# Kernel tuning notes

Hardware: AMD Instinct MI355X
Metric: run time of the kernel (lower is better)

The kernel has to match this reference:

```python
import jax, jax.numpy as jnp
import numpy as np

B, N, D = 8, 1024, 768
H = 12
HD = D // H  # 64
SCALE = HD ** (-0.5)


def setup_inputs() -> dict:
    key = jax.random.key(0)
    ks = jax.random.split(key, 11)
    s = 0.02
    return {
        "x": jax.random.normal(ks[0], (B, N, D), dtype=jnp.float32),
        "w_q": jax.random.normal(ks[1], (D, D), dtype=jnp.float32) * s,
        "b_q": jax.random.normal(ks[2], (D,), dtype=jnp.float32) * s,
        "w_k": jax.random.normal(ks[3], (D, D), dtype=jnp.float32) * s,
        "b_k": jax.random.normal(ks[4], (D,), dtype=jnp.float32) * s,
        "w_v": jax.random.normal(ks[5], (D, D), dtype=jnp.float32) * s,
        "b_v": jax.random.normal(ks[6], (D,), dtype=jnp.float32) * s,
        "w_qt": jax.random.normal(ks[7], (D, D), dtype=jnp.float32) * s,
        "b_qt": jax.random.normal(ks[8], (D,), dtype=jnp.float32) * s,
        "w_p": jax.random.normal(ks[9], (D, D), dtype=jnp.float32) * s,
        "b_p": jax.random.normal(ks[10], (D,), dtype=jnp.float32) * s,
    }


def _heads(y):
    # [B,N,D] -> [B,H,N,HD]
    b, n, d = y.shape
    return y.reshape(b, n, H, HD).transpose(0, 2, 1, 3)


def reference(x, w_q, b_q, w_k, b_k, w_v, b_v, w_qt, b_qt, w_p, b_p):
    # torch nn.Linear: y = x @ W.T + b
    q = _heads(x @ w_q.T + b_q)
    k = _heads(x @ w_k.T + b_k)
    v = _heads(x @ w_v.T + b_v)
    q_tilde = _heads(x @ w_qt.T + b_qt)
    # NOTE: source divides by self.scale = head_dim**-0.5 (i.e. multiplies by sqrt(hd)); reproduced faithfully
    corr = jnp.einsum("bhnd,bhmd->bhnm", q_tilde, k) / SCALE
    scores = jnp.einsum("bhnd,bhmd->bhnm", q, k) / SCALE + corr
    attn = jax.nn.softmax(scores, axis=-1)
    out = jnp.einsum("bhnm,bhmd->bhnd", attn, v)  # [B,H,N,HD]
    out = out.transpose(0, 2, 1, 3).reshape(x.shape[0], x.shape[1], D)
    out = out @ w_p.T + b_p
    return out, corr
```

## Files before the change

### kernel.cpp

```cpp
#include <hip/hip_runtime.h>

typedef __bf16 bf16_t;
typedef __bf16 bf16x8 __attribute__((ext_vector_type(8)));
typedef __bf16 bf16x4 __attribute__((ext_vector_type(4)));
typedef float f32x4 __attribute__((ext_vector_type(4)));

constexpr int BATCH = 8;
constexpr int NSEQ = 1024;
constexpr int DMODEL = 768;
constexpr int NH = 12;
constexpr int HDIM = 64;
constexpr int MROWS = BATCH * NSEQ;
constexpr int WSZ = DMODEL * DMODEL;
constexpr float L2E = 1.44269504088896f;

#define AS1(p) ((const __attribute__((address_space(1))) void*)(p))
#define AS3(p) ((__attribute__((address_space(3))) void*)(p))

__global__ __launch_bounds__(256) void prep_w(
    const float* __restrict__ wq, const float* __restrict__ wqt,
    const float* __restrict__ wk, const float* __restrict__ wv,
    const float* __restrict__ wp, const float* __restrict__ bq,
    const float* __restrict__ bqt, ushort* __restrict__ wb_,
    float* __restrict__ bqs)
{
    int i = blockIdx.x * 256 + threadIdx.x;
    bf16_t* w = (bf16_t*)wb_;
    float a = wq[i], b = wqt[i];
    w[i]            = (bf16_t)(a + b);
    w[WSZ + i]      = (bf16_t)b;
    w[2*WSZ + i]    = (bf16_t)wk[i];
    w[3*WSZ + i]    = (bf16_t)wv[i];
    w[4*WSZ + i]    = (bf16_t)wp[i];
    if (i < DMODEL) bqs[i] = bq[i] + bqt[i];
}

__global__ __launch_bounds__(256) void conv_x(const float* __restrict__ x,
                                              ushort* __restrict__ xb_)
{
    int i = (blockIdx.x * 256 + threadIdx.x) * 4;
    float4 v = *(const float4*)(x + i);
    bf16x4 r = { (bf16_t)v.x, (bf16_t)v.y, (bf16_t)v.z, (bf16_t)v.w };
    *(bf16x4*)((bf16_t*)xb_ + i) = r;
}

__device__ __forceinline__ void gemm_core(
    const bf16_t* __restrict__ A, const bf16_t* __restrict__ W,
    bf16_t* As, bf16_t* Bs, int m0, int n0, int tid, f32x4 acc[4][4])
{
    const int lane = tid & 63, wave = tid >> 6;
    const int g = lane >> 4, c = lane & 15;
    const int wm = wave >> 1, wn = wave & 1;

    const int r_b = tid >> 3;
    const int koff = 8 * ((tid & 7) ^ (r_b & 7));
    const size_t arow = (size_t)(m0 + r_b) * DMODEL + koff;
    const size_t brow = (size_t)(n0 + r_b) * DMODEL + koff;
    char* As_base = (char*)As + (tid & ~63) * 16;
    char* Bs_base = (char*)Bs + (tid & ~63) * 16;

    for (int k0 = 0; k0 < DMODEL; k0 += 64) {
        __syncthreads();
#pragma unroll
        for (int i = 0; i < 4; i++)
            __builtin_amdgcn_global_load_lds(
                AS1(A + arow + k0 + (size_t)i * 32 * DMODEL),
                AS3(As_base + i * 4096), 16, 0, 0);
#pragma unroll
        for (int i = 0; i < 4; i++)
            __builtin_amdgcn_global_load_lds(
                AS1(W + brow + k0 + (size_t)i * 32 * DMODEL),
                AS3(Bs_base + i * 4096), 16, 0, 0);
        __syncthreads();
#pragma unroll
        for (int kk = 0; kk < 2; kk++) {
            bf16x8 af[4], bfr[4];
#pragma unroll
            for (int mt = 0; mt < 4; mt++) {
                int r = wm * 64 + mt * 16 + c;
                af[mt] = *(const bf16x8*)(As + r * 64 + ((kk * 4 + g) ^ (r & 7)) * 8);
            }
#pragma unroll
            for (int nt = 0; nt < 4; nt++) {
                int r = wn * 64 + nt * 16 + c;
                bfr[nt] = *(const bf16x8*)(Bs + r * 64 + ((kk * 4 + g) ^ (r & 7)) * 8);
            }
#pragma unroll
            for (int mt = 0; mt < 4; mt++)
#pragma unroll
                for (int nt = 0; nt < 4; nt++)
                    acc[mt][nt] = __builtin_amdgcn_mfma_f32_16x16x32_bf16(
                        af[mt], bfr[nt], acc[mt][nt], 0, 0, 0);
        }
    }
}

__global__ __launch_bounds__(256) void gemm_qkv(
    const ushort* __restrict__ xb_, const ushort* __restrict__ wb_,
    const float* __restrict__ bqs, const float* __restrict__ bqt,
    const float* __restrict__ bk, const float* __restrict__ bv,
    ushort* __restrict__ o0, ushort* __restrict__ o1,
    ushort* __restrict__ o2, ushort* __restrict__ o3)
{
    __shared__ alignas(16) bf16_t As[128 * 64];
    __shared__ alignas(16) bf16_t Bs[128 * 64];
    const int bid = blockIdx.x;
    const int gid = (bid & 7) * 192 + (bid >> 3);
    const int z = gid / 384;
    const int rr = gid % 384;
    const int m0 = (rr / 6) * 128, n0 = (rr % 6) * 128;

    const bf16_t* A = (const bf16_t*)xb_;
    const bf16_t* W = (const bf16_t*)wb_ + (size_t)z * WSZ;
    const float* bias = (z == 0) ? bqs : (z == 1) ? bqt : (z == 2) ? bk : bv;
    bf16_t* outp = (bf16_t*)((z == 0) ? o0 : (z == 1) ? o1 : (z == 2) ? o2 : o3);
    f32x4 acc[4][4] = {};
    gemm_core(A, W, As, Bs, m0, n0, threadIdx.x, acc);

    const int tid = threadIdx.x, lane = tid & 63, wave = tid >> 6;
    const int g = lane >> 4, c = lane & 15;
    const int wm = wave >> 1, wn = wave & 1;
#pragma unroll
    for (int mt = 0; mt < 4; mt++)
#pragma unroll
        for (int nt = 0; nt < 4; nt++) {
            int col = n0 + wn * 64 + nt * 16 + c;
            int h = col >> 6, hd = col & 63;
            float bsv = bias[col];
#pragma unroll
            for (int j = 0; j < 4; j++) {
                int row = m0 + wm * 64 + mt * 16 + 4 * g + j;
                int b = row >> 10, ns = row & 1023;
                outp[(((size_t)b * NH + h) * NSEQ + ns) * HDIM + hd] =
                    (bf16_t)(acc[mt][nt][j] + bsv);
            }
        }
}

__global__ __launch_bounds__(256) void gemm_out(
    const ushort* __restrict__ ao_, const ushort* __restrict__ wp_,
    const float* __restrict__ bp, float* __restrict__ out)
{
    __shared__ alignas(16) bf16_t As[128 * 64];
    __shared__ alignas(16) bf16_t Bs[128 * 64];
    const int bid = blockIdx.x;
    const int gid = (bid & 7) * 48 + (bid >> 3);
    const int m0 = (gid / 6) * 128, n0 = (gid % 6) * 128;

    const bf16_t* A = (const bf16_t*)ao_;
    const bf16_t* W = (const bf16_t*)wp_;
    f32x4 acc[4][4] = {};
    gemm_core(A, W, As, Bs, m0, n0, threadIdx.x, acc);

    const int tid = threadIdx.x, lane = tid & 63, wave = tid >> 6;
    const int g = lane >> 4, c = lane & 15;
    const int wm = wave >> 1, wn = wave & 1;
#pragma unroll
    for (int mt = 0; mt < 4; mt++)
#pragma unroll
        for (int nt = 0; nt < 4; nt++) {
            int col = n0 + wn * 64 + nt * 16 + c;
            float bsv = bp[col];
#pragma unroll
            for (int j = 0; j < 4; j++) {
                int row = m0 + wm * 64 + mt * 16 + 4 * g + j;
                out[(size_t)row * DMODEL + col] = acc[mt][nt][j] + bsv;
            }
        }
}

__global__ __launch_bounds__(256) void attn_kernel(
    const ushort* __restrict__ qs_, const ushort* __restrict__ qt_,
    const ushort* __restrict__ kb_, const ushort* __restrict__ vb_,
    ushort* __restrict__ ao_, float* __restrict__ corr)
{
    __shared__ alignas(16) bf16_t VT[2][64 * 64];
    __shared__ alignas(16) bf16_t P[4][16 * 72];
    const bf16_t* QS = (const bf16_t*)qs_;
    const bf16_t* QT = (const bf16_t*)qt_;
    const bf16_t* Kb = (const bf16_t*)kb_;
    const bf16_t* Vb = (const bf16_t*)vb_;
    bf16_t* Ob = (bf16_t*)ao_;

    const int tid = threadIdx.x;
    const int w = tid >> 6, lane = tid & 63;
    const int g = lane >> 4, c = lane & 15;
    const int bid = blockIdx.x;
    const int gid = (bid & 7) * 192 + (bid >> 3);
    const int bh = gid >> 4, qb = gid & 15;
    const int q0 = qb * 64 + w * 16;
    const size_t base = (size_t)bh * (NSEQ * HDIM);

    bf16x8 qsf[2], qtf[2];
#pragma unroll
    for (int kk = 0; kk < 2; kk++) {
        qsf[kk] = *(const bf16x8*)(QS + base + (size_t)(q0 + c) * HDIM + kk * 32 + 8 * g);
        qtf[kk] = *(const bf16x8*)(QT + base + (size_t)(q0 + c) * HDIM + kk * 32 + 8 * g);
    }
    f32x4 oacc[4] = {};
    float mrun = -3e30f, lrun = 0.f;

    float* corr_b = corr + (size_t)bh * (NSEQ * NSEQ);
    float* corr_row = corr_b + (size_t)(q0 + c) * NSEQ + 4 * g;
    f32x4 ca_hold[4];

    for (int t = 0; t < 16; t++) {
        const int kv0 = t * 64;
        bf16_t* vt = VT[t & 1];
#pragma unroll
        for (int r2 = 0; r2 < 2; r2++) {
            const int hd0 = (r2 * 4 + w) * 8;
            bf16x8 vv = *(const bf16x8*)(Vb + base + (size_t)(kv0 + lane) * HDIM + hd0);
#pragma unroll
            for (int e = 0; e < 8; e++) {
                const int hd = hd0 + e;
                vt[hd * 64 + (lane ^ ((hd & 7) << 3))] = vv[e];
            }
        }
        bf16x8 kf[4][2];
#pragma unroll
        for (int kvt = 0; kvt < 4; kvt++) {
            const size_t krow = base + (size_t)(kv0 + kvt * 16 + c) * HDIM + 8 * g;
            kf[kvt][0] = *(const bf16x8*)(Kb + krow);
            kf[kvt][1] = *(const bf16x8*)(Kb + krow + 32);
        }
        if (t) {
#pragma unroll
            for (int kvt = 0; kvt < 4; kvt++)
                *(f32x4*)(corr_row + (kv0 - 64) + kvt * 16) = ca_hold[kvt];
        }
        f32x4 sv[4];
#pragma unroll
        for (int kvt = 0; kvt < 4; kvt++) {
            f32x4 sa = {0.f, 0.f, 0.f, 0.f};
            f32x4 ca = {0.f, 0.f, 0.f, 0.f};
            sa = __builtin_amdgcn_mfma_f32_16x16x32_bf16(kf[kvt][0], qsf[0], sa, 0, 0, 0);
            sa = __builtin_amdgcn_mfma_f32_16x16x32_bf16(kf[kvt][1], qsf[1], sa, 0, 0, 0);
            ca = __builtin_amdgcn_mfma_f32_16x16x32_bf16(kf[kvt][0], qtf[0], ca, 0, 0, 0);
            ca = __builtin_amdgcn_mfma_f32_16x16x32_bf16(kf[kvt][1], qtf[1], ca, 0, 0, 0);
            sv[kvt] = sa * 8.0f;
            ca_hold[kvt] = ca * 8.0f;
        }
        f32x4 mm;
#pragma unroll
        for (int j = 0; j < 4; j++)
            mm[j] = fmaxf(fmaxf(sv[0][j], sv[1][j]), fmaxf(sv[2][j], sv[3][j]));
        float tm = fmaxf(fmaxf(mm[0], mm[1]), fmaxf(mm[2], mm[3]));
        tm = fmaxf(tm, __shfl_xor(tm, 16));
        tm = fmaxf(tm, __shfl_xor(tm, 32));
        if (__any(tm > mrun + 8.0f)) {
            float newm = fmaxf(mrun, tm);
            float scl = exp2f((mrun - newm) * L2E);
            mrun = newm;
            lrun *= scl;
#pragma unroll
            for (int j = 0; j < 4; j++) {
                float scj = __shfl(scl, 4 * g + j);
#pragma unroll
                for (int nt = 0; nt < 4; nt++) oacc[nt][j] *= scj;
            }
        }
        float ps = 0.f;
#pragma unroll
        for (int kvt = 0; kvt < 4; kvt++)
#pragma unroll
            for (int j = 0; j < 4; j++) {
                float p = exp2f((sv[kvt][j] - mrun) * L2E);
                sv[kvt][j] = p;
                ps += p;
            }
        ps += __shfl_xor(ps, 16);
        ps += __shfl_xor(ps, 32);
        lrun += ps;
#pragma unroll
        for (int kvt = 0; kvt < 4; kvt++) {
            bf16x4 pb = { (bf16_t)sv[kvt][0], (bf16_t)sv[kvt][1],
                          (bf16_t)sv[kvt][2], (bf16_t)sv[kvt][3] };
            *(bf16x4*)(&P[w][c * 72 + kvt * 16 + 4 * g]) = pb;
        }
        asm volatile("s_waitcnt lgkmcnt(0)" ::: "memory");
        __builtin_amdgcn_sched_barrier(0);
        __builtin_amdgcn_s_barrier();
#pragma unroll
        for (int kk = 0; kk < 2; kk++) {
            bf16x8 pa = *(const bf16x8*)(&P[w][c * 72 + kk * 32 + 8 * g]);
#pragma unroll
            for (int nt = 0; nt < 4; nt++) {
                const int hd = nt * 16 + c;
                bf16x8 vf = *(const bf16x8*)(&vt[hd * 64 + ((kk * 32 + 8 * g) ^ ((hd & 7) << 3))]);
                oacc[nt] = __builtin_amdgcn_mfma_f32_16x16x32_bf16(pa, vf, oacc[nt], 0, 0, 0);
            }
        }
    }
#pragma unroll
    for (int kvt = 0; kvt < 4; kvt++)
        *(f32x4*)(corr_row + 960 + kvt * 16) = ca_hold[kvt];
    const int b = bh / NH, h = bh % NH;
    float lj[4];
#pragma unroll
    for (int j = 0; j < 4; j++) lj[j] = __shfl(lrun, 4 * g + j);
#pragma unroll
    for (int nt = 0; nt < 4; nt++)
#pragma unroll
        for (int j = 0; j < 4; j++) {
            float val = oacc[nt][j] / lj[j];
            Ob[(size_t)(b * NSEQ + q0 + 4 * g + j) * DMODEL + h * HDIM + nt * 16 + c] =
                (bf16_t)val;
        }
}

extern "C" void kernel_launch(void* const* d_in, const int* in_sizes, int n_in,
                              void* d_out, int out_size, void* d_ws, size_t ws_size,
                              hipStream_t stream)
{
    const float* x   = (const float*)d_in[0];
    const float* wq  = (const float*)d_in[1];
    const float* bq  = (const float*)d_in[2];
    const float* wk  = (const float*)d_in[3];
    const float* bk  = (const float*)d_in[4];
    const float* wv  = (const float*)d_in[5];
    const float* bv  = (const float*)d_in[6];
    const float* wqt = (const float*)d_in[7];
    const float* bqt = (const float*)d_in[8];
    const float* wp  = (const float*)d_in[9];
    const float* bp  = (const float*)d_in[10];

    char* ws = (char*)d_ws;
    ushort* xb  = (ushort*)(ws);
    ushort* wb  = (ushort*)(ws + 12582912);
    float*  bqs = (float*)(ws + 18481152);
    ushort* qs  = (ushort*)(ws + 18485248);
    ushort* qt  = qs + 6291456;
    ushort* kb  = qt + 6291456;
    ushort* vb  = kb + 6291456;
    ushort* ao  = vb + 6291456;

    float* out  = (float*)d_out;
    float* corr = out + (size_t)6291456;

    prep_w<<<2304, 256, 0, stream>>>(wq, wqt, wk, wv, wp, bq, bqt, wb, bqs);
    conv_x<<<6144, 256, 0, stream>>>(x, xb);
    gemm_qkv<<<1536, 256, 0, stream>>>(xb, wb, bqs, bqt, bk, bv, qs, qt, kb, vb);
    attn_kernel<<<1536, 256, 0, stream>>>(qs, qt, kb, vb, ao, corr);
    gemm_out<<<384, 256, 0, stream>>>(ao, wb + (size_t)4 * WSZ, bp, out);
}
```

Measured before the change: 256.4 us.

## Write V pre-transposed from QKV GEMM and load V fragments directly in attention

The QKV projection epilogue now writes V in a head-dim-major [B,H,HD,N] layout, using 4-wide bf16 vector stores. The attention kernel can then load V MFMA fragments straight from global memory into registers. This removes the per-tile shared-memory transpose of V and the block-wide barrier that guarded it. In exchange, each wave loads V itself with no sharing through LDS, which adds register pressure and redundant global/L2 traffic across the four waves.

```diff
diff --git a/kernel.cpp b/kernel.cpp
--- a/kernel.cpp
+++ b/kernel.cpp
@@ -127,12 +127,22 @@
             int col = n0 + wn * 64 + nt * 16 + c;
             int h = col >> 6, hd = col & 63;
             float bsv = bias[col];
-#pragma unroll
-            for (int j = 0; j < 4; j++) {
-                int row = m0 + wm * 64 + mt * 16 + 4 * g + j;
-                int b = row >> 10, ns = row & 1023;
-                outp[(((size_t)b * NH + h) * NSEQ + ns) * HDIM + hd] =
-                    (bf16_t)(acc[mt][nt][j] + bsv);
+            if (z == 3) {
+                int row0 = m0 + wm * 64 + mt * 16 + 4 * g;
+                int b = row0 >> 10, ns0 = row0 & 1023;
+                bf16x4 pb = { (bf16_t)(acc[mt][nt][0] + bsv),
+                              (bf16_t)(acc[mt][nt][1] + bsv),
+                              (bf16_t)(acc[mt][nt][2] + bsv),
+                              (bf16_t)(acc[mt][nt][3] + bsv) };
+                *(bf16x4*)(outp + ((size_t)(b * NH + h) * HDIM + hd) * NSEQ + ns0) = pb;
+            } else {
+#pragma unroll
+                for (int j = 0; j < 4; j++) {
+                    int row = m0 + wm * 64 + mt * 16 + 4 * g + j;
+                    int b = row >> 10, ns = row & 1023;
+                    outp[(((size_t)b * NH + h) * NSEQ + ns) * HDIM + hd] =
+                        (bf16_t)(acc[mt][nt][j] + bsv);
+                }
             }
         }
 }
@@ -171,15 +181,14 @@
 
 __global__ __launch_bounds__(256) void attn_kernel(
     const ushort* __restrict__ qs_, const ushort* __restrict__ qt_,
-    const ushort* __restrict__ kb_, const ushort* __restrict__ vb_,
+    const ushort* __restrict__ kb_, const ushort* __restrict__ vt_,
     ushort* __restrict__ ao_, float* __restrict__ corr)
 {
-    __shared__ alignas(16) bf16_t VT[2][64 * 64];
     __shared__ alignas(16) bf16_t P[4][16 * 72];
     const bf16_t* QS = (const bf16_t*)qs_;
     const bf16_t* QT = (const bf16_t*)qt_;
     const bf16_t* Kb = (const bf16_t*)kb_;
-    const bf16_t* Vb = (const bf16_t*)vb_;
+    const bf16_t* Vt = (const bf16_t*)vt_;
     bf16_t* Ob = (bf16_t*)ao_;
 
     const int tid = threadIdx.x;
@@ -206,17 +215,6 @@
 
     for (int t = 0; t < 16; t++) {
         const int kv0 = t * 64;
-        bf16_t* vt = VT[t & 1];
-#pragma unroll
-        for (int r2 = 0; r2 < 2; r2++) {
-            const int hd0 = (r2 * 4 + w) * 8;
-            bf16x8 vv = *(const bf16x8*)(Vb + base + (size_t)(kv0 + lane) * HDIM + hd0);
-#pragma unroll
-            for (int e = 0; e < 8; e++) {
-                const int hd = hd0 + e;
-                vt[hd * 64 + (lane ^ ((hd & 7) << 3))] = vv[e];
-            }
-        }
         bf16x8 kf[4][2];
 #pragma unroll
         for (int kvt = 0; kvt < 4; kvt++) {
@@ -224,6 +222,13 @@
             kf[kvt][0] = *(const bf16x8*)(Kb + krow);
             kf[kvt][1] = *(const bf16x8*)(Kb + krow + 32);
         }
+        bf16x8 vf[2][4];
+#pragma unroll
+        for (int kk = 0; kk < 2; kk++)
+#pragma unroll
+            for (int nt = 0; nt < 4; nt++)
+                vf[kk][nt] = *(const bf16x8*)(
+                    Vt + base + (size_t)(nt * 16 + c) * NSEQ + kv0 + kk * 32 + 8 * g);
         if (t) {
 #pragma unroll
             for (int kvt = 0; kvt < 4; kvt++)
@@ -278,18 +283,12 @@
                           (bf16_t)sv[kvt][2], (bf16_t)sv[kvt][3] };
             *(bf16x4*)(&P[w][c * 72 + kvt * 16 + 4 * g]) = pb;
         }
-        asm volatile("s_waitcnt lgkmcnt(0)" ::: "memory");
-        __builtin_amdgcn_sched_barrier(0);
-        __builtin_amdgcn_s_barrier();
 #pragma unroll
         for (int kk = 0; kk < 2; kk++) {
             bf16x8 pa = *(const bf16x8*)(&P[w][c * 72 + kk * 32 + 8 * g]);
 #pragma unroll
-            for (int nt = 0; nt < 4; nt++) {
-                const int hd = nt * 16 + c;
-                bf16x8 vf = *(const bf16x8*)(&vt[hd * 64 + ((kk * 32 + 8 * g) ^ ((hd & 7) << 3))]);
-                oacc[nt] = __builtin_amdgcn_mfma_f32_16x16x32_bf16(pa, vf, oacc[nt], 0, 0, 0);
-            }
+            for (int nt = 0; nt < 4; nt++)
+                oacc[nt] = __builtin_amdgcn_mfma_f32_16x16x32_bf16(pa, vf[kk][nt], oacc[nt], 0, 0, 0);
         }
     }
 #pragma unroll
@@ -332,15 +331,15 @@
     ushort* qs  = (ushort*)(ws + 18485248);
     ushort* qt  = qs + 6291456;
     ushort* kb  = qt + 6291456;
-    ushort* vb  = kb + 6291456;
-    ushort* ao  = vb + 6291456;
+    ushort* vt  = kb + 6291456;
+    ushort* ao  = vt + 6291456;
 
     float* out  = (float*)d_out;
     float* corr = out + (size_t)6291456;
 
     prep_w<<<2304, 256, 0, stream>>>(wq, wqt, wk, wv, wp, bq, bqt, wb, bqs);
     conv_x<<<6144, 256, 0, stream>>>(x, xb);
-    gemm_qkv<<<1536, 256, 0, stream>>>(xb, wb, bqs, bqt, bk, bv, qs, qt, kb, vb);
-    attn_kernel<<<1536, 256, 0, stream>>>(qs, qt, kb, vb, ao, corr);
+    gemm_qkv<<<1536, 256, 0, stream>>>(xb, wb, bqs, bqt, bk, bv, qs, qt, kb, vt);
+    attn_kernel<<<1536, 256, 0, stream>>>(qs, qt, kb, vt, ao, corr);
     gemm_out<<<384, 256, 0, stream>>>(ao, wb + (size_t)4 * WSZ, bp, out);
 }
```

Result: slower. 298.9 us (+16.6%).

## Split corr computation into separate kernel and fold scale into weights

Applied to the files above, without the earlier changes.

The corr QK^T product and its large fp32 store move out of the attention kernel into a standalone corr_kernel launched after the output projection. The factor of 8 (1/scale) is folded into the bf16 Q-sum and Q-tilde weights and biases, so both kernels skip the per-element multiply. The softmax exponent becomes a single FMA. This gives a leaner attention inner loop with fewer MFMAs and no interleaved global stores, at the cost of re-reading K in a second pass. It also adds bf16 rounding of the pre-scaled weights.

```diff
diff --git a/kernel.cpp b/kernel.cpp
--- a/kernel.cpp
+++ b/kernel.cpp
@@ -22,17 +22,20 @@
     const float* __restrict__ wk, const float* __restrict__ wv,
     const float* __restrict__ wp, const float* __restrict__ bq,
     const float* __restrict__ bqt, ushort* __restrict__ wb_,
-    float* __restrict__ bqs)
+    float* __restrict__ bqs, float* __restrict__ bqt8)
 {
     int i = blockIdx.x * 256 + threadIdx.x;
     bf16_t* w = (bf16_t*)wb_;
     float a = wq[i], b = wqt[i];
-    w[i]            = (bf16_t)(a + b);
-    w[WSZ + i]      = (bf16_t)b;
+    w[i]            = (bf16_t)(8.0f * (a + b));
+    w[WSZ + i]      = (bf16_t)(8.0f * b);
     w[2*WSZ + i]    = (bf16_t)wk[i];
     w[3*WSZ + i]    = (bf16_t)wv[i];
     w[4*WSZ + i]    = (bf16_t)wp[i];
-    if (i < DMODEL) bqs[i] = bq[i] + bqt[i];
+    if (i < DMODEL) {
+        bqs[i]  = 8.0f * (bq[i] + bqt[i]);
+        bqt8[i] = 8.0f * bqt[i];
+    }
 }
 
 __global__ __launch_bounds__(256) void conv_x(const float* __restrict__ x,
@@ -97,7 +100,7 @@
 
 __global__ __launch_bounds__(256) void gemm_qkv(
     const ushort* __restrict__ xb_, const ushort* __restrict__ wb_,
-    const float* __restrict__ bqs, const float* __restrict__ bqt,
+    const float* __restrict__ bqs, const float* __restrict__ bqt8,
     const float* __restrict__ bk, const float* __restrict__ bv,
     ushort* __restrict__ o0, ushort* __restrict__ o1,
     ushort* __restrict__ o2, ushort* __restrict__ o3)
@@ -112,7 +115,7 @@
 
     const bf16_t* A = (const bf16_t*)xb_;
     const bf16_t* W = (const bf16_t*)wb_ + (size_t)z * WSZ;
-    const float* bias = (z == 0) ? bqs : (z == 1) ? bqt : (z == 2) ? bk : bv;
+    const float* bias = (z == 0) ? bqs : (z == 1) ? bqt8 : (z == 2) ? bk : bv;
     bf16_t* outp = (bf16_t*)((z == 0) ? o0 : (z == 1) ? o1 : (z == 2) ? o2 : o3);
     f32x4 acc[4][4] = {};
     gemm_core(A, W, As, Bs, m0, n0, threadIdx.x, acc);
@@ -170,14 +173,12 @@
 }
 
 __global__ __launch_bounds__(256) void attn_kernel(
-    const ushort* __restrict__ qs_, const ushort* __restrict__ qt_,
-    const ushort* __restrict__ kb_, const ushort* __restrict__ vb_,
-    ushort* __restrict__ ao_, float* __restrict__ corr)
+    const ushort* __restrict__ qs_, const ushort* __restrict__ kb_,
+    const ushort* __restrict__ vb_, ushort* __restrict__ ao_)
 {
     __shared__ alignas(16) bf16_t VT[2][64 * 64];
     __shared__ alignas(16) bf16_t P[4][16 * 72];
     const bf16_t* QS = (const bf16_t*)qs_;
-    const bf16_t* QT = (const bf16_t*)qt_;
     const bf16_t* Kb = (const bf16_t*)kb_;
     const bf16_t* Vb = (const bf16_t*)vb_;
     bf16_t* Ob = (bf16_t*)ao_;
@@ -191,18 +192,13 @@
     const int q0 = qb * 64 + w * 16;
     const size_t base = (size_t)bh * (NSEQ * HDIM);
 
-    bf16x8 qsf[2], qtf[2];
-#pragma unroll
-    for (int kk = 0; kk < 2; kk++) {
+    bf16x8 qsf[2];
+#pragma unroll
+    for (int kk = 0; kk < 2; kk++)
         qsf[kk] = *(const bf16x8*)(QS + base + (size_t)(q0 + c) * HDIM + kk * 32 + 8 * g);
-        qtf[kk] = *(const bf16x8*)(QT + base + (size_t)(q0 + c) * HDIM + kk * 32 + 8 * g);
-    }
+
     f32x4 oacc[4] = {};
     float mrun = -3e30f, lrun = 0.f;
-
-    float* corr_b = corr + (size_t)bh * (NSEQ * NSEQ);
-    float* corr_row = corr_b + (size_t)(q0 + c) * NSEQ + 4 * g;
-    f32x4 ca_hold[4];
 
     for (int t = 0; t < 16; t++) {
         const int kv0 = t * 64;
@@ -224,22 +220,13 @@
             kf[kvt][0] = *(const bf16x8*)(Kb + krow);
             kf[kvt][1] = *(const bf16x8*)(Kb + krow + 32);
         }
-        if (t) {
-#pragma unroll
-            for (int kvt = 0; kvt < 4; kvt++)
-                *(f32x4*)(corr_row + (kv0 - 64) + kvt * 16) = ca_hold[kvt];
-        }
         f32x4 sv[4];
 #pragma unroll
         for (int kvt = 0; kvt < 4; kvt++) {
             f32x4 sa = {0.f, 0.f, 0.f, 0.f};
-            f32x4 ca = {0.f, 0.f, 0.f, 0.f};
             sa = __builtin_amdgcn_mfma_f32_16x16x32_bf16(kf[kvt][0], qsf[0], sa, 0, 0, 0);
             sa = __builtin_amdgcn_mfma_f32_16x16x32_bf16(kf[kvt][1], qsf[1], sa, 0, 0, 0);
-            ca = __builtin_amdgcn_mfma_f32_16x16x32_bf16(kf[kvt][0], qtf[0], ca, 0, 0, 0);
-            ca = __builtin_amdgcn_mfma_f32_16x16x32_bf16(kf[kvt][1], qtf[1], ca, 0, 0, 0);
-            sv[kvt] = sa * 8.0f;
-            ca_hold[kvt] = ca * 8.0f;
+            sv[kvt] = sa;
         }
         f32x4 mm;
 #pragma unroll
@@ -260,12 +247,13 @@
                 for (int nt = 0; nt < 4; nt++) oacc[nt][j] *= scj;
             }
         }
+        const float mneg = mrun * L2E;
         float ps = 0.f;
 #pragma unroll
         for (int kvt = 0; kvt < 4; kvt++)
 #pragma unroll
             for (int j = 0; j < 4; j++) {
-                float p = exp2f((sv[kvt][j] - mrun) * L2E);
+                float p = exp2f(__builtin_fmaf(sv[kvt][j], L2E, -mneg));
                 sv[kvt][j] = p;
                 ps += p;
             }
@@ -292,9 +280,6 @@
             }
         }
     }
-#pragma unroll
-    for (int kvt = 0; kvt < 4; kvt++)
-        *(f32x4*)(corr_row + 960 + kvt * 16) = ca_hold[kvt];
     const int b = bh / NH, h = bh % NH;
     float lj[4];
 #pragma unroll
@@ -307,6 +292,48 @@
             Ob[(size_t)(b * NSEQ + q0 + 4 * g + j) * DMODEL + h * HDIM + nt * 16 + c] =
                 (bf16_t)val;
         }
+}
+
+__global__ __launch_bounds__(256) void corr_kernel(
+    const ushort* __restrict__ qt_, const ushort* __restrict__ kb_,
+    float* __restrict__ corr)
+{
+    const bf16_t* QT = (const bf16_t*)qt_;
+    const bf16_t* Kb = (const bf16_t*)kb_;
+
+    const int tid = threadIdx.x;
+    const int w = tid >> 6, lane = tid & 63;
+    const int g = lane >> 4, c = lane & 15;
+    const int bid = blockIdx.x;
+    const int gid = (bid & 7) * 192 + (bid >> 3);
+    const int bh = gid >> 4, qb = gid & 15;
+    const int q0 = qb * 64 + w * 16;
+    const size_t base = (size_t)bh * (NSEQ * HDIM);
+
+    bf16x8 qtf[2];
+#pragma unroll
+    for (int kk = 0; kk < 2; kk++)
+        qtf[kk] = *(const bf16x8*)(QT + base + (size_t)(q0 + c) * HDIM + kk * 32 + 8 * g);
+
+    float* corr_row = corr + (size_t)bh * (NSEQ * NSEQ) + (size_t)(q0 + c) * NSEQ + 4 * g;
+
+    for (int t = 0; t < 16; t++) {
+        const int kv0 = t * 64;
+        bf16x8 kf[4][2];
+#pragma unroll
+        for (int kvt = 0; kvt < 4; kvt++) {
+            const size_t krow = base + (size_t)(kv0 + kvt * 16 + c) * HDIM + 8 * g;
+            kf[kvt][0] = *(const bf16x8*)(Kb + krow);
+            kf[kvt][1] = *(const bf16x8*)(Kb + krow + 32);
+        }
+#pragma unroll
+        for (int kvt = 0; kvt < 4; kvt++) {
+            f32x4 ca = {0.f, 0.f, 0.f, 0.f};
+            ca = __builtin_amdgcn_mfma_f32_16x16x32_bf16(kf[kvt][0], qtf[0], ca, 0, 0, 0);
+            ca = __builtin_amdgcn_mfma_f32_16x16x32_bf16(kf[kvt][1], qtf[1], ca, 0, 0, 0);
+            *(f32x4*)(corr_row + kv0 + kvt * 16) = ca;
+        }
+    }
 }
 
 extern "C" void kernel_launch(void* const* d_in, const int* in_sizes, int n_in,
@@ -326,21 +353,23 @@
     const float* bp  = (const float*)d_in[10];
 
     char* ws = (char*)d_ws;
-    ushort* xb  = (ushort*)(ws);
-    ushort* wb  = (ushort*)(ws + 12582912);
-    float*  bqs = (float*)(ws + 18481152);
-    ushort* qs  = (ushort*)(ws + 18485248);
-    ushort* qt  = qs + 6291456;
-    ushort* kb  = qt + 6291456;
-    ushort* vb  = kb + 6291456;
-    ushort* ao  = vb + 6291456;
+    ushort* xb   = (ushort*)(ws);
+    ushort* wb   = (ushort*)(ws + 12582912);
+    float*  bqs  = (float*)(ws + 18481152);
+    float*  bqt8 = (float*)(ws + 18485248);
+    ushort* qs   = (ushort*)(ws + 18489344);
+    ushort* qt   = qs + 6291456;
+    ushort* kb   = qt + 6291456;
+    ushort* vb   = kb + 6291456;
+    ushort* ao   = vb + 6291456;
 
     float* out  = (float*)d_out;
     float* corr = out + (size_t)6291456;
 
-    prep_w<<<2304, 256, 0, stream>>>(wq, wqt, wk, wv, wp, bq, bqt, wb, bqs);
+    prep_w<<<2304, 256, 0, stream>>>(wq, wqt, wk, wv, wp, bq, bqt, wb, bqs, bqt8);
     conv_x<<<6144, 256, 0, stream>>>(x, xb);
-    gemm_qkv<<<1536, 256, 0, stream>>>(xb, wb, bqs, bqt, bk, bv, qs, qt, kb, vb);
-    attn_kernel<<<1536, 256, 0, stream>>>(qs, qt, kb, vb, ao, corr);
+    gemm_qkv<<<1536, 256, 0, stream>>>(xb, wb, bqs, bqt8, bk, bv, qs, qt, kb, vb);
+    attn_kernel<<<1536, 256, 0, stream>>>(qs, kb, vb, ao);
     gemm_out<<<384, 256, 0, stream>>>(ao, wb + (size_t)4 * WSZ, bp, out);
-}
+    corr_kernel<<<1536, 256, 0, stream>>>(qt, kb, corr);
+}
```

New measurement: 324.0 us. 26.4% more time.
